# Optimization experiments

Hardware: AMD Instinct MI355X
Metric: run time of the kernel (lower is better)

## Reference

```python
import jax, jax.numpy as jnp
import numpy as np

# Channel schedule of FPSRefineNet(num_structure_points=64, in_channel=640, out=False):
# 640->512 (ReLU), 512->256 (ReLU), 256->128 (ReLU), 128->64 (ReLU since out=False)
CH = [640, 512, 256, 128, 64]
BN_EPS = 1e-5


def _conv_bn_relu(x, W, b, g, beta, m, v):
    # 1x1 Conv2d over [B,C,K,S] == channel matmul; BN in eval mode (running stats);
    # dropout is identity in eval.
    x = jnp.einsum('oc,bcks->boks', W, x) + b[None, :, None, None]
    inv = g / jnp.sqrt(v + BN_EPS)
    x = x * inv[None, :, None, None] + (beta - m * inv)[None, :, None, None]
    return jax.nn.relu(x)


def setup_inputs() -> dict:
    key = jax.random.key(0)
    ks = jax.random.split(key, 32)
    d = {}
    d['grouped_xyz'] = jax.random.normal(ks[0], (8, 3, 32, 1024), jnp.float32)
    d['grouped_points'] = jax.random.normal(ks[1], (8, 640, 32, 1024), jnp.float32)
    i = 2
    for li, (cin, cout) in enumerate(zip(CH[:-1], CH[1:])):
        d[f'W{li}'] = jax.random.normal(ks[i], (cout, cin), jnp.float32) / np.sqrt(cin).astype(np.float32); i += 1
        d[f'b{li}'] = jnp.zeros((cout,), jnp.float32)
        d[f'g{li}'] = jnp.ones((cout,), jnp.float32)
        d[f'beta{li}'] = jnp.zeros((cout,), jnp.float32)
        d[f'm{li}'] = 0.1 * jax.random.normal(ks[i], (cout,), jnp.float32); i += 1
        d[f'v{li}'] = 1.0 + 0.1 * jax.random.uniform(ks[i], (cout,), jnp.float32); i += 1
    return d


def reference(grouped_xyz, grouped_points,
              W0, b0, g0, beta0, m0, v0,
              W1, b1, g1, beta1, m1, v1,
              W2, b2, g2, beta2, m2, v2,
              W3, b3, g3, beta3, m3, v3):
    params = [(W0, b0, g0, beta0, m0, v0),
              (W1, b1, g1, beta1, m1, v1),
              (W2, b2, g2, beta2, m2, v2),
              (W3, b3, g3, beta3, m3, v3)]
    x = grouped_points  # [B, 640, K, S]
    for (W, b, g, be, m, v) in params:
        x = _conv_bn_relu(x, W, b, g, be, m, v)
    # softmax over K (dim=2)
    p = jax.nn.softmax(x, axis=2)  # [B, D'=64, K, S]
    # fused weighted sum over K: sum_k p[b,d,k,s]*xyz[b,c,k,s] -> [B, C, D', S]
    offset_xyz = jnp.einsum('bdks,bcks->bcds', p, grouped_xyz)
    return offset_xyz
```

## Files before the change

kernel.cpp:

```cpp
#include <hip/hip_runtime.h>

typedef unsigned short u16;
typedef __attribute__((ext_vector_type(8))) short bf16x8;
typedef __attribute__((ext_vector_type(4))) float f32x4;
typedef __attribute__((ext_vector_type(16))) float f32x16;

__device__ __forceinline__ u16 f2bf(float f) {
  union { float f; unsigned u; } x; x.f = f;
  return (u16)((x.u + 0x7FFFu + ((x.u >> 16) & 1u)) >> 16);
}
__device__ __forceinline__ float bf2f(u16 h) {
  union { unsigned u; float f; } x; x.u = ((unsigned)h) << 16; return x.f;
}


__global__ __launch_bounds__(256) void prep_kernel(
    const float* __restrict__ W0, const float* __restrict__ W1,
    const float* __restrict__ W2, const float* __restrict__ W3,
    const float* __restrict__ b0, const float* __restrict__ g0, const float* __restrict__ be0, const float* __restrict__ m0, const float* __restrict__ v0,
    const float* __restrict__ b1, const float* __restrict__ g1, const float* __restrict__ be1, const float* __restrict__ m1, const float* __restrict__ v1,
    const float* __restrict__ b2, const float* __restrict__ g2, const float* __restrict__ be2, const float* __restrict__ m2, const float* __restrict__ v2,
    const float* __restrict__ b3, const float* __restrict__ g3, const float* __restrict__ be3, const float* __restrict__ m3, const float* __restrict__ v3,
    u16* __restrict__ Wb, float* __restrict__ sc, float* __restrict__ sh)
{
  int i = blockIdx.x * 256 + threadIdx.x;
  if (i < 62464) {
    const float* Ws; int CIN, KS, local, dstb; bool f16 = false;
    if (i < 40960)      { local = i;         Ws = W0; CIN = 640; KS = 40; dstb = 0; }
    else if (i < 57344) { local = i - 40960; Ws = W1; CIN = 512; KS = 32; dstb = 327680; }
    else if (i < 61440) { local = i - 57344; Ws = W2; CIN = 256; KS = 16; dstb = 458752; }
    else                { local = i - 61440; Ws = W3; CIN = 128; KS = 4;  dstb = 491520; f16 = true; }
    int lane = local & 63, fi = local >> 6;
    int ks = fi % KS, mt = fi / KS;
    int row, k;
    if (!f16) { row = mt * 32 + (lane & 31); k = ks * 16 + (lane >> 5) * 8; }
    else      { row = mt * 16 + (lane & 15); k = ks * 32 + (lane >> 4) * 8; }
    const float* s = Ws + (size_t)row * CIN + k;
    bf16x8 pk;
    #pragma unroll
    for (int j = 0; j < 8; ++j) pk[j] = (short)f2bf(s[j]);
    *reinterpret_cast<bf16x8*>(Wb + dstb + (size_t)local * 8) = pk;
  }
  if (i < 960) {
    const float *B, *G, *BE, *M, *V; int c;
    if (i < 512)      { c = i;       B = b0; G = g0; BE = be0; M = m0; V = v0; }
    else if (i < 768) { c = i - 512; B = b1; G = g1; BE = be1; M = m1; V = v1; }
    else if (i < 896) { c = i - 768; B = b2; G = g2; BE = be2; M = m2; V = v2; }
    else              { c = i - 896; B = b3; G = g3; BE = be3; M = m3; V = v3; }
    float inv = G[c] / sqrtf(V[c] + 1e-5f);
    sc[i] = inv;
    sh[i] = (B[c] - M[c]) * inv + BE[c];
  }
}

template<int MT, int NT>
__device__ __forceinline__ void store_act32(f32x16 (&acc)[MT][NT],
    const float* __restrict__ sc, const float* __restrict__ sh,
    int mrow0, int ntb, int lane, u16* __restrict__ dst, int rowB)
{
  const int l31 = lane & 31, khalf = lane >> 5;
  #pragma unroll
  for (int mi = 0; mi < MT; ++mi) {
    #pragma unroll
    for (int rq = 0; rq < 4; ++rq) {
      const int ch0 = mrow0 + mi * 32 + rq * 8 + khalf * 4;
      const f32x4 s4 = *reinterpret_cast<const f32x4*>(sc + ch0);
      const f32x4 h4 = *reinterpret_cast<const f32x4*>(sh + ch0);
      #pragma unroll
      for (int nt = 0; nt < NT; ++nt) {
        const int px = (ntb + nt) * 32 + l31;
        float r0 = fmaxf(acc[mi][nt][rq * 4 + 0] * s4[0] + h4[0], 0.f);
        float r1 = fmaxf(acc[mi][nt][rq * 4 + 1] * s4[1] + h4[1], 0.f);
        float r2 = fmaxf(acc[mi][nt][rq * 4 + 2] * s4[2] + h4[2], 0.f);
        float r3 = fmaxf(acc[mi][nt][rq * 4 + 3] * s4[3] + h4[3], 0.f);
        uint2 pk;
        pk.x = (unsigned)f2bf(r0) | ((unsigned)f2bf(r1) << 16);
        pk.y = (unsigned)f2bf(r2) | ((unsigned)f2bf(r3) << 16);
        const unsigned byte = ((unsigned)(px * rowB + ch0 * 2)) ^ ((unsigned)((px & 7) << 4));
        *reinterpret_cast<uint2*>(reinterpret_cast<char*>(dst) + byte) = pk;
      }
    }
  }
}

__device__ __forceinline__ void load64(const float* __restrict__ gbase, int c, int w, float (&v)[8]) {
  const float* s = gbase + (size_t)(c * 64 + w * 8) * 32768u;
  #pragma unroll
  for (int kk = 0; kk < 8; ++kk) v[kk] = s[(size_t)kk * 32768u];
}
__device__ __forceinline__ void write64(float (&v)[8], char* __restrict__ buf, unsigned wb) {
  bf16x8 pk;
  #pragma unroll
  for (int kk = 0; kk < 8; ++kk) pk[kk] = (short)f2bf(v[kk]);
  *reinterpret_cast<bf16x8*>(buf + wb) = pk;
}

#define P0_MFMA(XB, c) { \
  __builtin_amdgcn_s_setprio(1); \
  _Pragma("unroll") \
  for (int ksl = 0; ksl < 4; ++ksl) { \
    const unsigned base = ((unsigned)(l31 * 128 + ksl * 32 + khalf * 16)) ^ sw; \
    bf16x8 bb0 = *reinterpret_cast<const bf16x8*>((XB) + base); \
    bf16x8 bb1 = *reinterpret_cast<const bf16x8*>((XB) + base + 4096); \
    acc0[0][0] = __builtin_amdgcn_mfma_f32_32x32x16_bf16(ar0[ksl & 1], bb0, acc0[0][0], 0, 0, 0); \
    acc0[0][1] = __builtin_amdgcn_mfma_f32_32x32x16_bf16(ar0[ksl & 1], bb1, acc0[0][1], 0, 0, 0); \
    acc0[1][0] = __builtin_amdgcn_mfma_f32_32x32x16_bf16(ar1[ksl & 1], bb0, acc0[1][0], 0, 0, 0); \
    acc0[1][1] = __builtin_amdgcn_mfma_f32_32x32x16_bf16(ar1[ksl & 1], bb1, acc0[1][1], 0, 0, 0); \
    const int g_ = (c) * 4 + ksl + 2; \
    if (g_ < 40) { \
      ar0[ksl & 1] = *reinterpret_cast<const bf16x8*>(A0 + g_ * 512); \
      ar1[ksl & 1] = *reinterpret_cast<const bf16x8*>(A1 + g_ * 512); \
    } \
  } \
  __builtin_amdgcn_s_setprio(0); \
}

__global__ __launch_bounds__(512, 4) void fused4_kernel(
    const float* __restrict__ gp, const u16* __restrict__ Wb,
    const float* __restrict__ sc, const float* __restrict__ sh,
    u16* __restrict__ x3)
{
  __shared__ u16 smem[40960];
  char* XsA = reinterpret_cast<char*>(smem);
  char* XsB = XsA + 8192;
  u16*  Y0s = smem + 8192;

  const int tid  = threadIdx.x;
  const int lane = tid & 63;
  const int w    = tid >> 6;
  const int l31  = lane & 31, khalf = lane >> 5;
  const unsigned sw = (unsigned)((l31 & 7) << 4);

  const int b  = blockIdx.x >> 9;
  const int jt = blockIdx.x & 511;
  const int j0 = jt << 6;

  const float* gbase = gp + (size_t)b * (640u * 32768u) + (unsigned)(j0 + lane);
  const unsigned wbyte = ((unsigned)(lane * 128 + w * 16)) ^ ((unsigned)((lane & 7) << 4));

  const u16* A0 = Wb + (size_t)(2 * w) * (40 * 512) + lane * 8;
  const u16* A1 = A0 + (size_t)(40 * 512);

  float vA[8], vB[8];
  bf16x8 ar0[2], ar1[2];
  f32x16 acc0[2][2] = {};

  load64(gbase, 0, w, vA);
  write64(vA, XsA, wbyte);
  load64(gbase, 1, w, vB);
  ar0[0] = *reinterpret_cast<const bf16x8*>(A0 + 0 * 512);
  ar1[0] = *reinterpret_cast<const bf16x8*>(A1 + 0 * 512);
  ar0[1] = *reinterpret_cast<const bf16x8*>(A0 + 1 * 512);
  ar1[1] = *reinterpret_cast<const bf16x8*>(A1 + 1 * 512);
  __syncthreads();

  #pragma unroll 1
  for (int c2 = 0; c2 < 5; ++c2) {
    const int ce = 2 * c2;
    {
      if (ce < 8) load64(gbase, ce + 2, w, vA);
      write64(vB, XsB, wbyte);
      P0_MFMA(XsA, ce);
      __syncthreads();
    }
    const int co = 2 * c2 + 1;
    {
      if (co < 8) load64(gbase, co + 2, w, vB);
      if (co < 9) write64(vA, XsA, wbyte);
      P0_MFMA(XsB, co);
      if (co < 9) __syncthreads();
    }
  }
  store_act32<2, 2>(acc0, sc, sh, w * 64, 0, lane, Y0s, 1024);
  __syncthreads();

  {
    f32x16 acc1[1][2] = {};
    const u16* A = Wb + 327680 + (size_t)w * (32 * 512) + lane * 8;
    bf16x8 ar8[8];
    #pragma unroll
    for (int q = 0; q < 8; ++q) ar8[q] = *reinterpret_cast<const bf16x8*>(A + q * 512);
    __builtin_amdgcn_s_setprio(1);
    #pragma unroll
    for (int ks = 0; ks < 32; ++ks) {
      const unsigned kb = (unsigned)(ks * 32 + khalf * 16);
      bf16x8 bb0 = *reinterpret_cast<const bf16x8*>(reinterpret_cast<const char*>(Y0s) + (((unsigned)(l31 * 1024) + kb) ^ sw));
      bf16x8 bb1 = *reinterpret_cast<const bf16x8*>(reinterpret_cast<const char*>(Y0s) + (((unsigned)((l31 + 32) * 1024) + kb) ^ sw));
      acc1[0][0] = __builtin_amdgcn_mfma_f32_32x32x16_bf16(ar8[ks & 7], bb0, acc1[0][0], 0, 0, 0);
      acc1[0][1] = __builtin_amdgcn_mfma_f32_32x32x16_bf16(ar8[ks & 7], bb1, acc1[0][1], 0, 0, 0);
      if (ks < 24) ar8[ks & 7] = *reinterpret_cast<const bf16x8*>(A + (ks + 8) * 512);
    }
    __builtin_amdgcn_s_setprio(0);
    __syncthreads();
    store_act32<1, 2>(acc1, sc + 512, sh + 512, w * 32, 0, lane, Y0s, 512);
    __syncthreads();
  }

  {
    f32x16 acc2[1][1] = {};
    const u16* A = Wb + 458752 + (size_t)(w & 3) * (16 * 512) + lane * 8;
    const int pxb = (w >> 2) * 32;
    bf16x8 ar8[8];
    #pragma unroll
    for (int q = 0; q < 8; ++q) ar8[q] = *reinterpret_cast<const bf16x8*>(A + q * 512);
    __builtin_amdgcn_s_setprio(1);
    #pragma unroll
    for (int ks = 0; ks < 16; ++ks) {
      const unsigned kb = (unsigned)(ks * 32 + khalf * 16);
      bf16x8 bb0 = *reinterpret_cast<const bf16x8*>(reinterpret_cast<const char*>(Y0s) + (((unsigned)((pxb + l31) * 512) + kb) ^ sw));
      acc2[0][0] = __builtin_amdgcn_mfma_f32_32x32x16_bf16(ar8[ks & 7], bb0, acc2[0][0], 0, 0, 0);
      if (ks < 8) ar8[ks & 7] = *reinterpret_cast<const bf16x8*>(A + (ks + 8) * 512);
    }
    __builtin_amdgcn_s_setprio(0);
    store_act32<1, 1>(acc2, sc + 768, sh + 768, (w & 3) * 32, w >> 2, lane, smem, 256);
    __syncthreads();
  }

  {
    const int r16 = lane & 15, g = lane >> 4;
    f32x4 acc3[2] = {};
    const u16* A = Wb + 491520 + (size_t)(w & 3) * (4 * 512) + lane * 8;
    bf16x8 a4[4];
    #pragma unroll
    for (int q = 0; q < 4; ++q) a4[q] = *reinterpret_cast<const bf16x8*>(A + q * 512);
    const int ntb = (w >> 2) * 2;
    __builtin_amdgcn_s_setprio(1);
    #pragma unroll
    for (int ks = 0; ks < 4; ++ks) {
      #pragma unroll
      for (int nt = 0; nt < 2; ++nt) {
        const int px = (ntb + nt) * 16 + r16;
        const unsigned byte = ((unsigned)(px * 256 + ks * 64 + g * 16)) ^ ((unsigned)((px & 7) << 4));
        bf16x8 bb = *reinterpret_cast<const bf16x8*>(reinterpret_cast<const char*>(smem) + byte);
        acc3[nt] = __builtin_amdgcn_mfma_f32_16x16x32_bf16(a4[ks], bb, acc3[nt], 0, 0, 0);
      }
    }
    __builtin_amdgcn_s_setprio(0);
    const int c0 = (w & 3) * 16 + g * 4;
    const f32x4 s4 = *reinterpret_cast<const f32x4*>(sc + 896 + c0);
    const f32x4 h4 = *reinterpret_cast<const f32x4*>(sh + 896 + c0);
    u16* x3b = x3 + ((size_t)b << 21) + j0;
    #pragma unroll
    for (int nt = 0; nt < 2; ++nt) {
      const int n = (ntb + nt) * 16 + r16;
      #pragma unroll
      for (int r = 0; r < 4; ++r) {
        float vv = fmaxf(acc3[nt][r] * s4[r] + h4[r], 0.f);
        x3b[(size_t)(c0 + r) * 32768 + n] = f2bf(vv);
      }
    }
  }
}

__global__ __launch_bounds__(256) void softmax_ws_kernel(
    const u16* __restrict__ x3, const float* __restrict__ xyz,
    float* __restrict__ out)
{
  const int tid = blockIdx.x * 256 + threadIdx.x;
  const int b = tid >> 15;
  const int rem = tid & 32767;
  const int d = rem >> 9;
  const int s0 = (rem & 511) * 2;

  const u16* xp = x3 + ((size_t)(b * 64 + d) << 15) + s0;
  float pa[32], pb[32];
  float mxa = -1e30f, mxb = -1e30f;
  #pragma unroll
  for (int k = 0; k < 32; ++k) {
    const unsigned u = *reinterpret_cast<const unsigned*>(xp + ((size_t)k << 10));
    const float va = bf2f((u16)(u & 0xFFFFu));
    const float vb = bf2f((u16)(u >> 16));
    pa[k] = va; pb[k] = vb;
    mxa = fmaxf(mxa, va); mxb = fmaxf(mxb, vb);
  }
  float sa = 0.f, sb = 0.f;
  #pragma unroll
  for (int k = 0; k < 32; ++k) {
    pa[k] = __expf(pa[k] - mxa); sa += pa[k];
    pb[k] = __expf(pb[k] - mxb); sb += pb[k];
  }
  const float inva = 1.0f / sa, invb = 1.0f / sb;

  const float* zp = xyz + (size_t)b * (3 * 32768) + s0;
  #pragma unroll
  for (int c = 0; c < 3; ++c) {
    float ax = 0.f, ay = 0.f;
    #pragma unroll
    for (int k = 0; k < 32; ++k) {
      const float2 z = *reinterpret_cast<const float2*>(zp + c * 32768 + (k << 10));
      ax += pa[k] * z.x; ay += pb[k] * z.y;
    }
    float2 o; o.x = ax * inva; o.y = ay * invb;
    *reinterpret_cast<float2*>(out + ((size_t)((b * 3 + c) * 64 + d) << 10) + s0) = o;
  }
}

extern "C" void kernel_launch(void* const* d_in, const int* in_sizes, int n_in,
                              void* d_out, int out_size, void* d_ws, size_t ws_size,
                              hipStream_t stream) {
  const float* xyz = (const float*)d_in[0];
  const float* gp  = (const float*)d_in[1];
  const float* W0 = (const float*)d_in[2];
  const float* W1 = (const float*)d_in[8];
  const float* W2 = (const float*)d_in[14];
  const float* W3 = (const float*)d_in[20];

  char* ws = (char*)d_ws;
  u16*   Wb = (u16*)ws;
  float* sc = (float*)(ws + 999424);
  float* sh = (float*)(ws + 1003264);
  u16*   x3 = (u16*)(ws + 1007104);

  prep_kernel<<<245, 256, 0, stream>>>(
      W0, W1, W2, W3,
      (const float*)d_in[3],  (const float*)d_in[4],  (const float*)d_in[5],  (const float*)d_in[6],  (const float*)d_in[7],
      (const float*)d_in[9],  (const float*)d_in[10], (const float*)d_in[11], (const float*)d_in[12], (const float*)d_in[13],
      (const float*)d_in[15], (const float*)d_in[16], (const float*)d_in[17], (const float*)d_in[18], (const float*)d_in[19],
      (const float*)d_in[21], (const float*)d_in[22], (const float*)d_in[23], (const float*)d_in[24], (const float*)d_in[25],
      Wb, sc, sh);

  fused4_kernel<<<4096, 512, 0, stream>>>(gp, Wb, sc, sh, x3);

  softmax_ws_kernel<<<1024, 256, 0, stream>>>(x3, xyz, (float*)d_out);
}
```

Baseline: 369.7 us.

## Deepen layer-0 K chunks to 128 channels and use packed bf16 conversion

Restructures the layer-0 pipeline to stage 128 input channels per buffer instead of 64. This halves the number of barrier-separated iterations from 10 to 5, and the LDS stores for the next chunk are split between two MFMA halves. It also swaps the manual round-to-nearest bf16 conversion for the hardware v_cvt_pk_bf16_f32 instruction, and shrinks shared memory from 80KB to 64KB by aliasing Y0s with the staging buffers. The cost is more live registers for two 8-float load sets per iteration, and the layer-2 output buffer has to move to a different smem offset.

```diff
diff --git a/kernel.cpp b/kernel.cpp
--- a/kernel.cpp
+++ b/kernel.cpp
@@ -11,6 +11,11 @@
 }
 __device__ __forceinline__ float bf2f(u16 h) {
   union { unsigned u; float f; } x; x.u = ((unsigned)h) << 16; return x.f;
+}
+__device__ __forceinline__ unsigned cvtpk(float lo, float hi) {
+  unsigned r;
+  asm("v_cvt_pk_bf16_f32 %0, %1, %2" : "=v"(r) : "v"(lo), "v"(hi));
+  return r;
 }
 
 
@@ -74,8 +79,8 @@
         float r2 = fmaxf(acc[mi][nt][rq * 4 + 2] * s4[2] + h4[2], 0.f);
         float r3 = fmaxf(acc[mi][nt][rq * 4 + 3] * s4[3] + h4[3], 0.f);
         uint2 pk;
-        pk.x = (unsigned)f2bf(r0) | ((unsigned)f2bf(r1) << 16);
-        pk.y = (unsigned)f2bf(r2) | ((unsigned)f2bf(r3) << 16);
+        pk.x = cvtpk(r0, r1);
+        pk.y = cvtpk(r2, r3);
         const unsigned byte = ((unsigned)(px * rowB + ch0 * 2)) ^ ((unsigned)((px & 7) << 4));
         *reinterpret_cast<uint2*>(reinterpret_cast<char*>(dst) + byte) = pk;
       }
@@ -83,33 +88,37 @@
   }
 }
 
-__device__ __forceinline__ void load64(const float* __restrict__ gbase, int c, int w, float (&v)[8]) {
-  const float* s = gbase + (size_t)(c * 64 + w * 8) * 32768u;
+__device__ __forceinline__ void load8(const float* __restrict__ gbase, int choff, float (&v)[8]) {
+  const float* s = gbase + (size_t)choff * 32768u;
   #pragma unroll
   for (int kk = 0; kk < 8; ++kk) v[kk] = s[(size_t)kk * 32768u];
 }
-__device__ __forceinline__ void write64(float (&v)[8], char* __restrict__ buf, unsigned wb) {
-  bf16x8 pk;
-  #pragma unroll
-  for (int kk = 0; kk < 8; ++kk) pk[kk] = (short)f2bf(v[kk]);
-  *reinterpret_cast<bf16x8*>(buf + wb) = pk;
-}
-
-#define P0_MFMA(XB, c) { \
+__device__ __forceinline__ void write8(float (&v)[8], char* __restrict__ buf, unsigned wb) {
+  uint4 pk;
+  pk.x = cvtpk(v[0], v[1]);
+  pk.y = cvtpk(v[2], v[3]);
+  pk.z = cvtpk(v[4], v[5]);
+  pk.w = cvtpk(v[6], v[7]);
+  *reinterpret_cast<uint4*>(buf + wb) = pk;
+}
+
+#define P0_HALF(XB, c, ks0) { \
   __builtin_amdgcn_s_setprio(1); \
   _Pragma("unroll") \
   for (int ksl = 0; ksl < 4; ++ksl) { \
-    const unsigned base = ((unsigned)(l31 * 128 + ksl * 32 + khalf * 16)) ^ sw; \
+    const int ks = (ks0) + ksl; \
+    const unsigned base = ((unsigned)(l31 * 256 + ks * 32 + khalf * 16)) ^ sw; \
     bf16x8 bb0 = *reinterpret_cast<const bf16x8*>((XB) + base); \
-    bf16x8 bb1 = *reinterpret_cast<const bf16x8*>((XB) + base + 4096); \
-    acc0[0][0] = __builtin_amdgcn_mfma_f32_32x32x16_bf16(ar0[ksl & 1], bb0, acc0[0][0], 0, 0, 0); \
-    acc0[0][1] = __builtin_amdgcn_mfma_f32_32x32x16_bf16(ar0[ksl & 1], bb1, acc0[0][1], 0, 0, 0); \
-    acc0[1][0] = __builtin_amdgcn_mfma_f32_32x32x16_bf16(ar1[ksl & 1], bb0, acc0[1][0], 0, 0, 0); \
-    acc0[1][1] = __builtin_amdgcn_mfma_f32_32x32x16_bf16(ar1[ksl & 1], bb1, acc0[1][1], 0, 0, 0); \
-    const int g_ = (c) * 4 + ksl + 2; \
+    bf16x8 bb1 = *reinterpret_cast<const bf16x8*>((XB) + base + 8192); \
+    const int slot = ks & 1; \
+    acc0[0][0] = __builtin_amdgcn_mfma_f32_32x32x16_bf16(ar0[slot], bb0, acc0[0][0], 0, 0, 0); \
+    acc0[0][1] = __builtin_amdgcn_mfma_f32_32x32x16_bf16(ar0[slot], bb1, acc0[0][1], 0, 0, 0); \
+    acc0[1][0] = __builtin_amdgcn_mfma_f32_32x32x16_bf16(ar1[slot], bb0, acc0[1][0], 0, 0, 0); \
+    acc0[1][1] = __builtin_amdgcn_mfma_f32_32x32x16_bf16(ar1[slot], bb1, acc0[1][1], 0, 0, 0); \
+    const int g_ = (c) * 8 + ks + 2; \
     if (g_ < 40) { \
-      ar0[ksl & 1] = *reinterpret_cast<const bf16x8*>(A0 + g_ * 512); \
-      ar1[ksl & 1] = *reinterpret_cast<const bf16x8*>(A1 + g_ * 512); \
+      ar0[slot] = *reinterpret_cast<const bf16x8*>(A0 + g_ * 512); \
+      ar1[slot] = *reinterpret_cast<const bf16x8*>(A1 + g_ * 512); \
     } \
   } \
   __builtin_amdgcn_s_setprio(0); \
@@ -120,10 +129,10 @@
     const float* __restrict__ sc, const float* __restrict__ sh,
     u16* __restrict__ x3)
 {
-  __shared__ u16 smem[40960];
+  __shared__ u16 smem[32768];
   char* XsA = reinterpret_cast<char*>(smem);
-  char* XsB = XsA + 8192;
-  u16*  Y0s = smem + 8192;
+  char* XsB = XsA + 16384;
+  u16*  Y0s = smem;
 
   const int tid  = threadIdx.x;
   const int lane = tid & 63;
@@ -136,7 +145,8 @@
   const int j0 = jt << 6;
 
   const float* gbase = gp + (size_t)b * (640u * 32768u) + (unsigned)(j0 + lane);
-  const unsigned wbyte = ((unsigned)(lane * 128 + w * 16)) ^ ((unsigned)((lane & 7) << 4));
+  const unsigned wbH0 = ((unsigned)(lane * 256 + w * 16)) ^ ((unsigned)((lane & 7) << 4));
+  const unsigned wbH1 = wbH0 + 128;
 
   const u16* A0 = Wb + (size_t)(2 * w) * (40 * 512) + lane * 8;
   const u16* A1 = A0 + (size_t)(40 * 512);
@@ -145,32 +155,31 @@
   bf16x8 ar0[2], ar1[2];
   f32x16 acc0[2][2] = {};
 
-  load64(gbase, 0, w, vA);
-  write64(vA, XsA, wbyte);
-  load64(gbase, 1, w, vB);
+  load8(gbase, 0 * 128 + 0 * 64 + w * 8, vA);
+  load8(gbase, 0 * 128 + 1 * 64 + w * 8, vB);
   ar0[0] = *reinterpret_cast<const bf16x8*>(A0 + 0 * 512);
   ar1[0] = *reinterpret_cast<const bf16x8*>(A1 + 0 * 512);
   ar0[1] = *reinterpret_cast<const bf16x8*>(A0 + 1 * 512);
   ar1[1] = *reinterpret_cast<const bf16x8*>(A1 + 1 * 512);
+  write8(vA, XsA, wbH0);
+  write8(vB, XsA, wbH1);
   __syncthreads();
 
   #pragma unroll 1
-  for (int c2 = 0; c2 < 5; ++c2) {
-    const int ce = 2 * c2;
-    {
-      if (ce < 8) load64(gbase, ce + 2, w, vA);
-      write64(vB, XsB, wbyte);
-      P0_MFMA(XsA, ce);
-      __syncthreads();
-    }
-    const int co = 2 * c2 + 1;
-    {
-      if (co < 8) load64(gbase, co + 2, w, vB);
-      if (co < 9) write64(vA, XsA, wbyte);
-      P0_MFMA(XsB, co);
-      if (co < 9) __syncthreads();
-    }
-  }
+  for (int c = 0; c < 5; ++c) {
+    char* bufc = (c & 1) ? XsB : XsA;
+    char* bufn = (c & 1) ? XsA : XsB;
+    if (c < 4) {
+      load8(gbase, (c + 1) * 128 + 0 * 64 + w * 8, vA);
+      load8(gbase, (c + 1) * 128 + 1 * 64 + w * 8, vB);
+    }
+    P0_HALF(bufc, c, 0);
+    if (c < 4) write8(vA, bufn, wbH0);
+    P0_HALF(bufc, c, 4);
+    if (c < 4) write8(vB, bufn, wbH1);
+    __syncthreads();
+  }
+
   store_act32<2, 2>(acc0, sc, sh, w * 64, 0, lane, Y0s, 1024);
   __syncthreads();
 
@@ -212,7 +221,7 @@
       if (ks < 8) ar8[ks & 7] = *reinterpret_cast<const bf16x8*>(A + (ks + 8) * 512);
     }
     __builtin_amdgcn_s_setprio(0);
-    store_act32<1, 1>(acc2, sc + 768, sh + 768, (w & 3) * 32, w >> 2, lane, smem, 256);
+    store_act32<1, 1>(acc2, sc + 768, sh + 768, (w & 3) * 32, w >> 2, lane, smem + 16384, 256);
     __syncthreads();
   }
 
@@ -231,7 +240,7 @@
       for (int nt = 0; nt < 2; ++nt) {
         const int px = (ntb + nt) * 16 + r16;
         const unsigned byte = ((unsigned)(px * 256 + ks * 64 + g * 16)) ^ ((unsigned)((px & 7) << 4));
-        bf16x8 bb = *reinterpret_cast<const bf16x8*>(reinterpret_cast<const char*>(smem) + byte);
+        bf16x8 bb = *reinterpret_cast<const bf16x8*>(reinterpret_cast<const char*>(smem) + 32768 + byte);
         acc3[nt] = __builtin_amdgcn_mfma_f32_16x16x32_bf16(a4[ks], bb, acc3[nt], 0, 0, 0);
       }
     }
```

Result: no change. 362.8 us (-1.9%).
